# Kernel tuning notes

Hardware: AMD Instinct MI355X
Metric: run time of the kernel (lower is better)

## Reference

```python
import jax, jax.numpy as jnp
import numpy as np

B, M, E, H = 256, 196, 1024, 8
Dh = E // H          # 128 = att_mid_dim[0]
MID = 64             # att_mid_dim[1]
ALPHA = 1.3          # CELU alpha
EPS = 1e-5


def group_norm(x, w, b, groups=H, eps=EPS):
    # x: [N, C]; torch GroupNorm over channel groups
    N, C = x.shape
    xg = x.reshape(N, groups, C // groups)
    mu = xg.mean(-1, keepdims=True)
    var = xg.var(-1, keepdims=True)
    xn = ((xg - mu) * jax.lax.rsqrt(var + eps)).reshape(N, C)
    return xn * w + b


def proj(x, W, b, gw, gb):
    # Linear -> CELU(1.3) -> GroupNorm(H)
    return group_norm(jax.nn.celu(x @ W + b, alpha=ALPHA), gw, gb)


def setup_inputs() -> dict:
    key0 = jax.random.key(0)
    ks = jax.random.split(key0, 16)
    d = {}
    d["query"] = jax.random.normal(ks[0], (B, E), jnp.float32)
    d["key"] = jax.random.normal(ks[1], (B, M, E), jnp.float32)
    d["mask"] = jax.random.randint(ks[2], (B, M), 0, 2, jnp.int32)
    d["value1"] = jax.random.normal(ks[3], (B, E), jnp.float32)
    d["value2"] = jax.random.normal(ks[4], (B, M, E), jnp.float32)
    s = 0.02
    for i, nm in enumerate(["q", "k", "v1", "v2"]):
        d[f"W{nm}"] = jax.random.normal(ks[5 + i], (E, E), jnp.float32) * s
        d[f"b{nm}"] = jnp.zeros((E,), jnp.float32)
        d[f"g{nm}_w"] = jnp.ones((E,), jnp.float32)
        d[f"g{nm}_b"] = jnp.zeros((E,), jnp.float32)
    d["Wb"] = jax.random.normal(ks[9], (Dh, MID), jnp.float32) * s
    d["bb"] = jnp.zeros((MID,), jnp.float32)
    d["Ws"] = jax.random.normal(ks[10], (MID, 1), jnp.float32) * s
    d["bs"] = jnp.zeros((1,), jnp.float32)
    d["Wc"] = jax.random.normal(ks[11], (MID, Dh), jnp.float32) * s
    d["bc"] = jnp.zeros((Dh,), jnp.float32)
    return d


def reference(query, key, mask, value1, value2,
              Wq, bq, gq_w, gq_b, Wk, bk, gk_w, gk_b,
              Wv1, bv1, gv1_w, gv1_b, Wv2, bv2, gv2_w, gv2_b,
              Wb, bb, Ws, bs, Wc, bc):
    # input projections (dropout layers are identity at eval)
    q = proj(query, Wq, bq, gq_w, gq_b).reshape(B, H, Dh)
    v1 = proj(value1, Wv1, bv1, gv1_w, gv1_b).reshape(B, H, Dh)
    k = proj(key.reshape(-1, E), Wk, bk, gk_w, gk_b).reshape(B, M, H, Dh).transpose(0, 2, 1, 3)   # [B,H,M,Dh]
    v2 = proj(value2.reshape(-1, E), Wv2, bv2, gv2_w, gv2_b).reshape(B, M, H, Dh).transpose(0, 2, 1, 3)

    # SCAttDec
    att_map = q[:, :, None, :] * k                                # [B,H,M,Dh]
    hidden = jax.nn.relu(att_map @ Wb + bb)                       # [B,H,M,MID]
    maskf = mask.astype(hidden.dtype)                             # [B,M]
    mext = maskf[:, None, :, None]                                # [B,1,M,1]
    att_map_pool = jnp.sum(hidden * mext, axis=2) / jnp.sum(mext, axis=2)   # [B,H,MID]

    alpha_spatial = (hidden @ Ws + bs)[..., 0]                    # [B,H,M]
    alpha_spatial = jnp.where(mask[:, None, :] == 0, -1e9, alpha_spatial)
    alpha_spatial = jax.nn.softmax(alpha_spatial, axis=-1)
    v2_pooled = jnp.einsum("bhm,bhmd->bhd", alpha_spatial, v2)    # [B,H,Dh]

    alpha_channel = jax.nn.sigmoid(att_map_pool @ Wc + bc)        # [B,H,Dh]
    attn = v1 * v2_pooled * alpha_channel                         # [B,H,Dh]
    return attn.reshape(B, H * Dh)
```

## Files before the change

kernel.cpp:

```cpp
#include <hip/hip_runtime.h>

typedef unsigned short u16;
typedef unsigned int u32;
typedef unsigned long long u64;
typedef __attribute__((ext_vector_type(8))) short short8;
typedef __attribute__((ext_vector_type(4))) float floatx4;

#define E_ 1024
#define B_ 256
#define M_ 196
#define H_ 8
#define DH_ 128
#define MID_ 64
#define NKROW 50176

__device__ __forceinline__ u16 f2bf(float f){
  union { float f; u32 u; } v; v.f = f;
  return (u16)((v.u + (((v.u >> 16) & 1u) + 0x7fffu)) >> 16);
}
__device__ __forceinline__ float bf2f(u16 h){
  union { u32 u; float f; } v; v.u = ((u32)h) << 16;
  return v.f;
}
__device__ __forceinline__ u32 pack_bf2(float a, float b){
  u32 ua = __float_as_uint(a) + 0x8000u;
  u32 ub = __float_as_uint(b) + 0x8000u;
  return __builtin_amdgcn_perm(ub, ua, 0x07060302);
}
__device__ __forceinline__ void gl_lds16(const void* g, void* l){
  __builtin_amdgcn_global_load_lds(
      (const __attribute__((address_space(1))) u32*)g,
      (__attribute__((address_space(3))) u32*)l, 16, 0, 0);
}

__global__ __launch_bounds__(256) void xconv_kernel(
    float* __restrict__ key, float* __restrict__ value2,
    float* __restrict__ query, float* __restrict__ value1)
{
  int gr = blockIdx.x * 8 + (threadIdx.x >> 5);
  int i  = threadIdx.x & 31;
  float* X; int r;
  if (gr < NKROW)               { X = key;    r = gr; }
  else if (gr < 2*NKROW)        { X = value2; r = gr - NKROW; }
  else if (gr < 2*NKROW + B_)   { X = query;  r = gr - 2*NKROW; }
  else                          { X = value1; r = gr - 2*NKROW - B_; }
  const float4* src = (const float4*)(X + (size_t)r * E_) + i * 8;
  float4 v[8];
  #pragma unroll
  for (int j = 0; j < 8; j++) v[j] = src[j];
  __syncthreads();
  uint4 o[4];
  #pragma unroll
  for (int j = 0; j < 4; j++){
    o[j].x = pack_bf2(v[2*j].x,   v[2*j].y);
    o[j].y = pack_bf2(v[2*j].z,   v[2*j].w);
    o[j].z = pack_bf2(v[2*j+1].x, v[2*j+1].y);
    o[j].w = pack_bf2(v[2*j+1].z, v[2*j+1].w);
  }
  uint4* dst = (uint4*)((u16*)X + (size_t)r * 2048) + i * 4;
  #pragma unroll
  for (int j = 0; j < 4; j++) dst[j] = o[j];
}

__global__ __launch_bounds__(256) void wconv_kernel(
    const float* __restrict__ Wq, const float* __restrict__ Wk,
    const float* __restrict__ Wv1, const float* __restrict__ Wv2,
    u16* __restrict__ Wt)
{
  __shared__ u16 tile[64][72];
  const float* W = (blockIdx.z == 0) ? Wq : (blockIdx.z == 1) ? Wk
                 : (blockIdx.z == 2) ? Wv1 : Wv2;
  u16* out = Wt + (size_t)blockIdx.z * (E_ * E_);
  int k0 = blockIdx.x * 64, c0 = blockIdx.y * 64;
  int tx = threadIdx.x & 63, ty = threadIdx.x >> 6;
  #pragma unroll
  for (int i = 0; i < 16; i++){
    int k = ty * 16 + i;
    tile[k][tx] = f2bf(W[(size_t)(k0 + k) * E_ + c0 + tx]);
  }
  __syncthreads();
  #pragma unroll
  for (int i = 0; i < 16; i++){
    int c = ty * 16 + i;
    out[(size_t)(c0 + c) * E_ + k0 + tx] = tile[tx][c];
  }
}

__global__ __launch_bounds__(256) void proj_kernel(
    const u16* __restrict__ xq_, const u16* __restrict__ xk_,
    const u16* __restrict__ xv1_, const u16* __restrict__ xv2_,
    const float* __restrict__ bq, const float* __restrict__ gqw, const float* __restrict__ gqb,
    const float* __restrict__ bk, const float* __restrict__ gkw, const float* __restrict__ gkb,
    const float* __restrict__ bv1, const float* __restrict__ gv1w, const float* __restrict__ gv1b,
    const float* __restrict__ bv2, const float* __restrict__ gv2w, const float* __restrict__ gv2b,
    const u16* __restrict__ Wt,
    u16* __restrict__ qout, u16* __restrict__ khead,
    u16* __restrict__ v1out, u16* __restrict__ v2head)
{
  __shared__ __align__(16) u16 a_lds[128 * 64];
  __shared__ __align__(16) u16 b_lds[128 * 64];
  __shared__ float s_sum[256];
  __shared__ float s_sq[256];

  const int tid = threadIdx.x;
  const int w = tid >> 6, lane = tid & 63, qd = lane >> 4, lr = lane & 15;
  const int rh = w >> 1, ch = w & 1;

  const int mtb = blockIdx.y;
  const u16* X; const float *bias, *gw, *gb; u16* outp; int row0, matsel, hm;
  if (mtb < 392)      { X = xk_;  bias = bk;  gw = gkw;  gb = gkb;  outp = khead;  row0 = mtb*128;        matsel = 1; hm = 1; }
  else if (mtb < 784) { X = xv2_; bias = bv2; gw = gv2w; gb = gv2b; outp = v2head; row0 = (mtb-392)*128;  matsel = 3; hm = 1; }
  else if (mtb < 786) { X = xq_;  bias = bq;  gw = gqw;  gb = gqb;  outp = qout;   row0 = (mtb-784)*128;  matsel = 0; hm = 0; }
  else                { X = xv1_; bias = bv1; gw = gv1w; gb = gv1b; outp = v1out;  row0 = (mtb-786)*128;  matsel = 2; hm = 0; }
  const int hsel = blockIdx.x, col0 = hsel * 128;

  const int sl = lane & 7, sr = lane >> 3, swc = sl ^ sr;
  const u16* aptr = X + (size_t)(row0 + w*32 + sr) * 2048 + swc * 8;
  const u16* bptr = Wt + (size_t)matsel * (E_*E_) + (size_t)(col0 + w*32 + sr) * E_ + swc * 8;

  floatx4 acc[4][4];
  #pragma unroll
  for (int i = 0; i < 4; i++)
    #pragma unroll
    for (int j = 0; j < 4; j++){
      floatx4 z = {0.f, 0.f, 0.f, 0.f};
      acc[i][j] = z;
    }

  for (int kt = 0; kt < 16; kt++){
    __syncthreads();
    #pragma unroll
    for (int c = 0; c < 4; c++)
      gl_lds16(aptr + (size_t)c*8*2048 + kt*64, &a_lds[(w*32 + c*8)*64]);
    #pragma unroll
    for (int c = 0; c < 4; c++)
      gl_lds16(bptr + (size_t)c*8*E_ + kt*64, &b_lds[(w*32 + c*8)*64]);
    __syncthreads();
    #pragma unroll
    for (int ks = 0; ks < 2; ks++){
      const int slot = ((ks*4 + qd) ^ (lr & 7)) * 8;
      short8 afr[4], bfr[4];
      #pragma unroll
      for (int m2 = 0; m2 < 4; m2++)
        afr[m2] = *(const short8*)&a_lds[(rh*64 + m2*16 + lr)*64 + slot];
      #pragma unroll
      for (int nt = 0; nt < 4; nt++)
        bfr[nt] = *(const short8*)&b_lds[(ch*64 + nt*16 + lr)*64 + slot];
      #pragma unroll
      for (int m2 = 0; m2 < 4; m2++)
        #pragma unroll
        for (int nt = 0; nt < 4; nt++)
          acc[m2][nt] = __builtin_amdgcn_mfma_f32_16x16x32_bf16(afr[m2], bfr[nt], acc[m2][nt], 0, 0, 0);
    }
  }

  float biasv[4], gwv[4], gbv[4];
  #pragma unroll
  for (int nt = 0; nt < 4; nt++){
    int c = col0 + ch*64 + nt*16 + lr;
    biasv[nt] = bias[c]; gwv[nt] = gw[c]; gbv[nt] = gb[c];
  }
  #pragma unroll
  for (int m2 = 0; m2 < 4; m2++){
    #pragma unroll
    for (int r = 0; r < 4; r++){
      float s = 0.f, s2 = 0.f;
      #pragma unroll
      for (int nt = 0; nt < 4; nt++){
        float x = acc[m2][nt][r] + biasv[nt];
        x = (x > 0.f) ? x : 1.3f * expm1f(x * (1.0f / 1.3f));
        acc[m2][nt][r] = x;
        s += x; s2 += x * x;
      }
      #pragma unroll
      for (int off = 1; off < 16; off <<= 1){
        s  += __shfl_xor(s,  off, 64);
        s2 += __shfl_xor(s2, off, 64);
      }
      if (lr == 0){
        int row = rh*64 + m2*16 + qd*4 + r;
        s_sum[row*2 + ch] = s;
        s_sq [row*2 + ch] = s2;
      }
    }
  }
  __syncthreads();
  #pragma unroll
  for (int m2 = 0; m2 < 4; m2++){
    #pragma unroll
    for (int r = 0; r < 4; r++){
      int row = rh*64 + m2*16 + qd*4 + r;
      float s  = s_sum[row*2] + s_sum[row*2 + 1];
      float s2 = s_sq [row*2] + s_sq [row*2 + 1];
      float mean = s * 0.0078125f;
      float var  = s2 * 0.0078125f - mean * mean;
      float rstd = rsqrtf(var + 1e-5f);
      u32 rg = row0 + row;
      size_t base;
      if (hm){
        u32 bi = (u32)(((u64)rg * 171197ull) >> 25);
        u32 m  = rg - bi * 196u;
        base = ((size_t)(bi*H_ + hsel)*M_ + m) * DH_ + ch*64;
      } else {
        base = (size_t)rg * E_ + col0 + ch*64;
      }
      #pragma unroll
      for (int nt = 0; nt < 4; nt++)
        outp[base + nt*16 + lr] = f2bf((acc[m2][nt][r] - mean) * rstd * gwv[nt] + gbv[nt]);
    }
  }
}

__global__ __launch_bounds__(256) void attn_kernel(
    const u16* __restrict__ qproj, const u16* __restrict__ khead,
    const u16* __restrict__ v1proj, const u16* __restrict__ v2head,
    const int* __restrict__ mask,
    const float* __restrict__ Wb, const float* __restrict__ bb,
    const float* __restrict__ Ws, const float* __restrict__ bs,
    const float* __restrict__ Wc, const float* __restrict__ bc,
    float* __restrict__ outp)
{
  __shared__ u16 wbt[64 * 136];
  __shared__ float qv[128];
  __shared__ float mrow[208];
  __shared__ float logitv[208];
  __shared__ float hsum_l[4][64];
  __shared__ float wexpv[208];
  __shared__ float poolv[64];
  __shared__ float v2acc[4][128];
  __shared__ float red[8];

  const int tid = threadIdx.x;
  const int w = tid >> 6, lane = tid & 63, qd = lane >> 4, lr = lane & 15;
  const int b = blockIdx.y, h = blockIdx.x;

  const u16* kbase  = khead  + (size_t)(b*H_ + h) * (M_*DH_);
  const u16* v2base = v2head + (size_t)(b*H_ + h) * (M_*DH_);

  if (tid < 128) qv[tid] = bf2f(qproj[(size_t)b * E_ + h * DH_ + tid]);
  if (tid < 208) mrow[tid] = (tid < M_) ? (float)mask[b * M_ + tid] : 0.f;
  __syncthreads();

  {
    int n = tid & 63, kb = (tid >> 6) * 32;
    #pragma unroll
    for (int kk = 0; kk < 32; kk++)
      wbt[n * 136 + kb + kk] = f2bf(qv[kb + kk] * Wb[(kb + kk) * MID_ + n]);
  }
  __syncthreads();

  float wsv[4], bbv[4];
  #pragma unroll
  for (int nt = 0; nt < 4; nt++){ wsv[nt] = Ws[nt * 16 + lr]; bbv[nt] = bb[nt * 16 + lr]; }
  const float bsv = bs[0];
  float hs[4] = {0, 0, 0, 0};

  for (int mt = w; mt < 13; mt += 4){
    int mrow_g = mt * 16 + lr;
    int mcl = (mrow_g < M_) ? mrow_g : (M_ - 1);
    const u16* arow = kbase + (size_t)mcl * DH_;
    floatx4 hacc[4];
    #pragma unroll
    for (int nt = 0; nt < 4; nt++){ floatx4 z = {0.f, 0.f, 0.f, 0.f}; hacc[nt] = z; }
    #pragma unroll
    for (int kc = 0; kc < 4; kc++){
      short8 afr = *(const short8*)(arow + kc * 32 + qd * 8);
      #pragma unroll
      for (int nt = 0; nt < 4; nt++){
        short8 bfr = *(const short8*)&wbt[(nt * 16 + lr) * 136 + kc * 32 + qd * 8];
        hacc[nt] = __builtin_amdgcn_mfma_f32_16x16x32_bf16(afr, bfr, hacc[nt], 0, 0, 0);
      }
    }
    float lp[4] = {0, 0, 0, 0};
    #pragma unroll
    for (int nt = 0; nt < 4; nt++){
      #pragma unroll
      for (int r = 0; r < 4; r++){
        float hv = hacc[nt][r] + bbv[nt];
        hv = fmaxf(hv, 0.f);
        lp[r] += hv * wsv[nt];
        hs[nt] += mrow[mt * 16 + qd * 4 + r] * hv;
      }
    }
    #pragma unroll
    for (int r = 0; r < 4; r++){
      float a = lp[r];
      #pragma unroll
      for (int off = 1; off < 16; off <<= 1) a += __shfl_xor(a, off, 64);
      if (lr == 0) logitv[mt * 16 + qd * 4 + r] = a + bsv;
    }
  }
  #pragma unroll
  for (int nt = 0; nt < 4; nt++){
    hs[nt] += __shfl_xor(hs[nt], 16, 64);
    hs[nt] += __shfl_xor(hs[nt], 32, 64);
  }
  if (lane < 16){
    #pragma unroll
    for (int nt = 0; nt < 4; nt++) hsum_l[w][nt * 16 + lane] = hs[nt];
  }
  __syncthreads();

  if (w == 0){
    float s = 0.f;
    for (int m = lane; m < M_; m += 64) s += mrow[m];
    #pragma unroll
    for (int off = 1; off < 64; off <<= 1) s += __shfl_xor(s, off, 64);
    if (lane == 0) red[0] = s;
  } else if (w == 1){
    float mx = -1e30f;
    for (int m = lane; m < M_; m += 64) if (mrow[m] > 0.5f) mx = fmaxf(mx, logitv[m]);
    #pragma unroll
    for (int off = 1; off < 64; off <<= 1) mx = fmaxf(mx, __shfl_xor(mx, off, 64));
    if (lane == 0) red[1] = mx;
  } else if (w == 2){
    poolv[lane & 63] = hsum_l[0][lane & 63] + hsum_l[1][lane & 63]
                     + hsum_l[2][lane & 63] + hsum_l[3][lane & 63];
  }
  __syncthreads();
  const float cnt = red[0], mx = red[1];
  if (tid < 208)
    wexpv[tid] = (tid < M_ && mrow[tid] > 0.5f) ? expf(logitv[tid] - mx) : 0.f;
  __syncthreads();
  if (w == 0){
    float s = 0.f;
    for (int m = lane; m < M_; m += 64) s += wexpv[m];
    #pragma unroll
    for (int off = 1; off < 64; off <<= 1) s += __shfl_xor(s, off, 64);
    if (lane == 0) red[2] = s;
  } else if (w == 1){
    poolv[lane & 63] = poolv[lane & 63] / cnt;
  }
  __syncthreads();
  const float S = red[2];

  {
    float ac[8] = {0, 0, 0, 0, 0, 0, 0, 0};
    #pragma unroll
    for (int it = 0; it < 13; it++){
      int m = it * 16 + w * 4 + qd;
      if (m < M_){
        float we = wexpv[m];
        uint4 u = *(const uint4*)(v2base + (size_t)m * DH_ + lr * 8);
        ac[0] += we * bf2f((u16)(u.x & 0xffff));
        ac[1] += we * bf2f((u16)(u.x >> 16));
        ac[2] += we * bf2f((u16)(u.y & 0xffff));
        ac[3] += we * bf2f((u16)(u.y >> 16));
        ac[4] += we * bf2f((u16)(u.z & 0xffff));
        ac[5] += we * bf2f((u16)(u.z >> 16));
        ac[6] += we * bf2f((u16)(u.w & 0xffff));
        ac[7] += we * bf2f((u16)(u.w >> 16));
      }
    }
    #pragma unroll
    for (int j = 0; j < 8; j++){
      ac[j] += __shfl_xor(ac[j], 16, 64);
      ac[j] += __shfl_xor(ac[j], 32, 64);
    }
    if (qd == 0){
      #pragma unroll
      for (int j = 0; j < 8; j++) v2acc[w][lr * 8 + j] = ac[j];
    }
  }
  __syncthreads();

  if (tid < 128){
    float a = 0.f;
    #pragma unroll 8
    for (int j = 0; j < 64; j++) a += poolv[j] * Wc[j * DH_ + tid];
    float acv = 1.f / (1.f + expf(-(a + bc[tid])));
    float vp = (v2acc[0][tid] + v2acc[1][tid] + v2acc[2][tid] + v2acc[3][tid]) / S;
    float o = bf2f(v1proj[(size_t)b * E_ + h * DH_ + tid]) * vp * acv;
    outp[(size_t)b * E_ + h * DH_ + tid] = o;
  }
}

extern "C" void kernel_launch(void* const* d_in, const int* in_sizes, int n_in,
                              void* d_out, int out_size, void* d_ws, size_t ws_size,
                              hipStream_t stream)
{
  float* query  = (float*)d_in[0];
  float* key    = (float*)d_in[1];
  const int* mask = (const int*)d_in[2];
  float* value1 = (float*)d_in[3];
  float* value2 = (float*)d_in[4];
  const float* Wq  = (const float*)d_in[5];
  const float* bq  = (const float*)d_in[6];
  const float* gqw = (const float*)d_in[7];
  const float* gqb = (const float*)d_in[8];
  const float* Wk  = (const float*)d_in[9];
  const float* bk  = (const float*)d_in[10];
  const float* gkw = (const float*)d_in[11];
  const float* gkb = (const float*)d_in[12];
  const float* Wv1 = (const float*)d_in[13];
  const float* bv1 = (const float*)d_in[14];
  const float* gv1w= (const float*)d_in[15];
  const float* gv1b= (const float*)d_in[16];
  const float* Wv2 = (const float*)d_in[17];
  const float* bv2 = (const float*)d_in[18];
  const float* gv2w= (const float*)d_in[19];
  const float* gv2b= (const float*)d_in[20];
  const float* Wb  = (const float*)d_in[21];
  const float* bb  = (const float*)d_in[22];
  const float* Ws  = (const float*)d_in[23];
  const float* bs  = (const float*)d_in[24];
  const float* Wc  = (const float*)d_in[25];
  const float* bc  = (const float*)d_in[26];

  const size_t NHD = (size_t)B_ * H_ * M_ * DH_;
  u16* khead  = (u16*)d_ws;
  u16* v2head = khead  + NHD;
  u16* qout   = v2head + NHD;
  u16* v1out  = qout   + (size_t)B_ * E_;
  u16* Wt     = v1out  + (size_t)B_ * E_;

  xconv_kernel<<<(2*NKROW + 2*B_)/8, 256, 0, stream>>>(key, value2, query, value1);

  dim3 g0(16, 16, 4);
  wconv_kernel<<<g0, 256, 0, stream>>>(Wq, Wk, Wv1, Wv2, Wt);

  dim3 g1(8, 788);
  proj_kernel<<<g1, 256, 0, stream>>>(
      (const u16*)query, (const u16*)key, (const u16*)value1, (const u16*)value2,
      bq, gqw, gqb, bk, gkw, gkb, bv1, gv1w, gv1b, bv2, gv2w, gv2b,
      Wt, qout, khead, v1out, v2head);

  dim3 g2(H_, B_);
  attn_kernel<<<g2, 256, 0, stream>>>(qout, khead, v1out, v2head, mask,
      Wb, bb, Ws, bs, Wc, bc, (float*)d_out);
}
```

Before: 1.020 ms.

## Enlarge projection GEMM tile to 256x256 with double-buffered LDS prefetch

The projection GEMM moves from 128x128 tiles with 256 threads to 256x256 tiles with 512 threads. K steps of 32 now use double-buffered LDS, so the next tile's global-to-LDS load overlaps the current MFMAs, and each wave owns a full 128-column head, which removes the cross-wave LDS reduction for GroupNorm. This is meant to raise data reuse per loaded byte and hide load latency, at the cost of more accumulator registers per thread. The other changes are smaller: the xconv loads are made coalesced, CELU and the softmax/sigmoid exponentials use fast __expf, and the Wc matvec is split across all 256 threads.

```diff
diff --git a/kernel.cpp b/kernel.cpp
--- a/kernel.cpp
+++ b/kernel.cpp
@@ -31,6 +31,10 @@
   __builtin_amdgcn_global_load_lds(
       (const __attribute__((address_space(1))) u32*)g,
       (__attribute__((address_space(3))) u32*)l, 16, 0, 0);
+}
+__device__ __forceinline__ float celu_f(float x){
+  float xn = 1.3f * (__expf(x * 0.76923076923f) - 1.0f);
+  return x > 0.f ? x : xn;
 }
 
 __global__ __launch_bounds__(256) void xconv_kernel(
@@ -44,22 +48,19 @@
   else if (gr < 2*NKROW)        { X = value2; r = gr - NKROW; }
   else if (gr < 2*NKROW + B_)   { X = query;  r = gr - 2*NKROW; }
   else                          { X = value1; r = gr - 2*NKROW - B_; }
-  const float4* src = (const float4*)(X + (size_t)r * E_) + i * 8;
+  const float4* src = (const float4*)(X + (size_t)r * E_);
   float4 v[8];
   #pragma unroll
-  for (int j = 0; j < 8; j++) v[j] = src[j];
-  __syncthreads();
-  uint4 o[4];
-  #pragma unroll
-  for (int j = 0; j < 4; j++){
-    o[j].x = pack_bf2(v[2*j].x,   v[2*j].y);
-    o[j].y = pack_bf2(v[2*j].z,   v[2*j].w);
-    o[j].z = pack_bf2(v[2*j+1].x, v[2*j+1].y);
-    o[j].w = pack_bf2(v[2*j+1].z, v[2*j+1].w);
-  }
-  uint4* dst = (uint4*)((u16*)X + (size_t)r * 2048) + i * 4;
-  #pragma unroll
-  for (int j = 0; j < 4; j++) dst[j] = o[j];
+  for (int j = 0; j < 8; j++) v[j] = src[j * 32 + i];
+  __syncthreads();
+  uint2* dst = (uint2*)((u16*)X + (size_t)r * 2048);
+  #pragma unroll
+  for (int j = 0; j < 8; j++){
+    uint2 o;
+    o.x = pack_bf2(v[j].x, v[j].y);
+    o.y = pack_bf2(v[j].z, v[j].w);
+    dst[j * 32 + i] = o;
+  }
 }
 
 __global__ __launch_bounds__(256) void wconv_kernel(
@@ -86,7 +87,7 @@
   }
 }
 
-__global__ __launch_bounds__(256) void proj_kernel(
+__global__ __launch_bounds__(512, 2) void proj_kernel(
     const u16* __restrict__ xq_, const u16* __restrict__ xk_,
     const u16* __restrict__ xv1_, const u16* __restrict__ xv2_,
     const float* __restrict__ bq, const float* __restrict__ gqw, const float* __restrict__ gqb,
@@ -97,78 +98,83 @@
     u16* __restrict__ qout, u16* __restrict__ khead,
     u16* __restrict__ v1out, u16* __restrict__ v2head)
 {
-  __shared__ __align__(16) u16 a_lds[128 * 64];
-  __shared__ __align__(16) u16 b_lds[128 * 64];
-  __shared__ float s_sum[256];
-  __shared__ float s_sq[256];
+  __shared__ __align__(16) u16 a_lds[2][256 * 32];
+  __shared__ __align__(16) u16 b_lds[2][256 * 32];
 
   const int tid = threadIdx.x;
   const int w = tid >> 6, lane = tid & 63, qd = lane >> 4, lr = lane & 15;
-  const int rh = w >> 1, ch = w & 1;
-
-  const int mtb = blockIdx.y;
+  const int wm = w & 3, wn = w >> 2;
+
+  const int mtb = blockIdx.x;
   const u16* X; const float *bias, *gw, *gb; u16* outp; int row0, matsel, hm;
-  if (mtb < 392)      { X = xk_;  bias = bk;  gw = gkw;  gb = gkb;  outp = khead;  row0 = mtb*128;        matsel = 1; hm = 1; }
-  else if (mtb < 784) { X = xv2_; bias = bv2; gw = gv2w; gb = gv2b; outp = v2head; row0 = (mtb-392)*128;  matsel = 3; hm = 1; }
-  else if (mtb < 786) { X = xq_;  bias = bq;  gw = gqw;  gb = gqb;  outp = qout;   row0 = (mtb-784)*128;  matsel = 0; hm = 0; }
-  else                { X = xv1_; bias = bv1; gw = gv1w; gb = gv1b; outp = v1out;  row0 = (mtb-786)*128;  matsel = 2; hm = 0; }
-  const int hsel = blockIdx.x, col0 = hsel * 128;
-
-  const int sl = lane & 7, sr = lane >> 3, swc = sl ^ sr;
-  const u16* aptr = X + (size_t)(row0 + w*32 + sr) * 2048 + swc * 8;
-  const u16* bptr = Wt + (size_t)matsel * (E_*E_) + (size_t)(col0 + w*32 + sr) * E_ + swc * 8;
-
-  floatx4 acc[4][4];
+  if (mtb < 196)      { X = xk_;  bias = bk;  gw = gkw;  gb = gkb;  outp = khead;  row0 = mtb*256;        matsel = 1; hm = 1; }
+  else if (mtb < 392) { X = xv2_; bias = bv2; gw = gv2w; gb = gv2b; outp = v2head; row0 = (mtb-196)*256;  matsel = 3; hm = 1; }
+  else if (mtb == 392){ X = xq_;  bias = bq;  gw = gqw;  gb = gqb;  outp = qout;   row0 = 0;              matsel = 0; hm = 0; }
+  else                { X = xv1_; bias = bv1; gw = gv1w; gb = gv1b; outp = v1out;  row0 = 0;              matsel = 2; hm = 0; }
+  const int cp = blockIdx.y, col0 = cp * 256;
+
+  const int srow = lane >> 2, sslot = lane & 3, sswz = sslot ^ (srow & 3);
+  const u16* aptr0 = X + (size_t)(row0 + (w*2    )*16 + srow) * 2048 + sswz * 8;
+  const u16* aptr1 = X + (size_t)(row0 + (w*2 + 1)*16 + srow) * 2048 + sswz * 8;
+  const u16* wbase = Wt + (size_t)matsel * (E_*E_);
+  const u16* bptr0 = wbase + (size_t)(col0 + (w*2    )*16 + srow) * E_ + sswz * 8;
+  const u16* bptr1 = wbase + (size_t)(col0 + (w*2 + 1)*16 + srow) * E_ + sswz * 8;
+
+  floatx4 acc[4][8];
   #pragma unroll
   for (int i = 0; i < 4; i++)
     #pragma unroll
-    for (int j = 0; j < 4; j++){
+    for (int j = 0; j < 8; j++){
       floatx4 z = {0.f, 0.f, 0.f, 0.f};
       acc[i][j] = z;
     }
 
-  for (int kt = 0; kt < 16; kt++){
+  gl_lds16(aptr0, &a_lds[0][(w*2    )*16*32]);
+  gl_lds16(aptr1, &a_lds[0][(w*2 + 1)*16*32]);
+  gl_lds16(bptr0, &b_lds[0][(w*2    )*16*32]);
+  gl_lds16(bptr1, &b_lds[0][(w*2 + 1)*16*32]);
+  __syncthreads();
+
+  const int fslot = (qd ^ (lr & 3)) * 8;
+  for (int kt = 0; kt < 32; kt++){
+    const int cur = kt & 1, nxt = cur ^ 1;
+    if (kt < 31){
+      const int ko = (kt + 1) * 32;
+      gl_lds16(aptr0 + ko, &a_lds[nxt][(w*2    )*16*32]);
+      gl_lds16(aptr1 + ko, &a_lds[nxt][(w*2 + 1)*16*32]);
+      gl_lds16(bptr0 + ko, &b_lds[nxt][(w*2    )*16*32]);
+      gl_lds16(bptr1 + ko, &b_lds[nxt][(w*2 + 1)*16*32]);
+    }
+    short8 afr[4], bfr[8];
+    #pragma unroll
+    for (int m2 = 0; m2 < 4; m2++)
+      afr[m2] = *(const short8*)&a_lds[cur][(wm*64 + m2*16 + lr)*32 + fslot];
+    #pragma unroll
+    for (int nt = 0; nt < 8; nt++)
+      bfr[nt] = *(const short8*)&b_lds[cur][(wn*128 + nt*16 + lr)*32 + fslot];
+    #pragma unroll
+    for (int m2 = 0; m2 < 4; m2++)
+      #pragma unroll
+      for (int nt = 0; nt < 8; nt++)
+        acc[m2][nt] = __builtin_amdgcn_mfma_f32_16x16x32_bf16(afr[m2], bfr[nt], acc[m2][nt], 0, 0, 0);
     __syncthreads();
-    #pragma unroll
-    for (int c = 0; c < 4; c++)
-      gl_lds16(aptr + (size_t)c*8*2048 + kt*64, &a_lds[(w*32 + c*8)*64]);
-    #pragma unroll
-    for (int c = 0; c < 4; c++)
-      gl_lds16(bptr + (size_t)c*8*E_ + kt*64, &b_lds[(w*32 + c*8)*64]);
-    __syncthreads();
-    #pragma unroll
-    for (int ks = 0; ks < 2; ks++){
-      const int slot = ((ks*4 + qd) ^ (lr & 7)) * 8;
-      short8 afr[4], bfr[4];
-      #pragma unroll
-      for (int m2 = 0; m2 < 4; m2++)
-        afr[m2] = *(const short8*)&a_lds[(rh*64 + m2*16 + lr)*64 + slot];
-      #pragma unroll
-      for (int nt = 0; nt < 4; nt++)
-        bfr[nt] = *(const short8*)&b_lds[(ch*64 + nt*16 + lr)*64 + slot];
-      #pragma unroll
-      for (int m2 = 0; m2 < 4; m2++)
-        #pragma unroll
-        for (int nt = 0; nt < 4; nt++)
-          acc[m2][nt] = __builtin_amdgcn_mfma_f32_16x16x32_bf16(afr[m2], bfr[nt], acc[m2][nt], 0, 0, 0);
-    }
-  }
-
-  float biasv[4], gwv[4], gbv[4];
-  #pragma unroll
-  for (int nt = 0; nt < 4; nt++){
-    int c = col0 + ch*64 + nt*16 + lr;
+  }
+
+  float biasv[8], gwv[8], gbv[8];
+  #pragma unroll
+  for (int nt = 0; nt < 8; nt++){
+    int c = col0 + wn*128 + nt*16 + lr;
     biasv[nt] = bias[c]; gwv[nt] = gw[c]; gbv[nt] = gb[c];
   }
+  const int head = cp*2 + wn;
   #pragma unroll
   for (int m2 = 0; m2 < 4; m2++){
     #pragma unroll
     for (int r = 0; r < 4; r++){
       float s = 0.f, s2 = 0.f;
       #pragma unroll
-      for (int nt = 0; nt < 4; nt++){
-        float x = acc[m2][nt][r] + biasv[nt];
-        x = (x > 0.f) ? x : 1.3f * expm1f(x * (1.0f / 1.3f));
+      for (int nt = 0; nt < 8; nt++){
+        float x = celu_f(acc[m2][nt][r] + biasv[nt]);
         acc[m2][nt][r] = x;
         s += x; s2 += x * x;
       }
@@ -177,35 +183,20 @@
         s  += __shfl_xor(s,  off, 64);
         s2 += __shfl_xor(s2, off, 64);
       }
-      if (lr == 0){
-        int row = rh*64 + m2*16 + qd*4 + r;
-        s_sum[row*2 + ch] = s;
-        s_sq [row*2 + ch] = s2;
-      }
-    }
-  }
-  __syncthreads();
-  #pragma unroll
-  for (int m2 = 0; m2 < 4; m2++){
-    #pragma unroll
-    for (int r = 0; r < 4; r++){
-      int row = rh*64 + m2*16 + qd*4 + r;
-      float s  = s_sum[row*2] + s_sum[row*2 + 1];
-      float s2 = s_sq [row*2] + s_sq [row*2 + 1];
       float mean = s * 0.0078125f;
       float var  = s2 * 0.0078125f - mean * mean;
       float rstd = rsqrtf(var + 1e-5f);
-      u32 rg = row0 + row;
+      u32 rg = row0 + wm*64 + m2*16 + qd*4 + r;
       size_t base;
       if (hm){
         u32 bi = (u32)(((u64)rg * 171197ull) >> 25);
         u32 m  = rg - bi * 196u;
-        base = ((size_t)(bi*H_ + hsel)*M_ + m) * DH_ + ch*64;
+        base = ((size_t)(bi*H_ + head)*M_ + m) * DH_;
       } else {
-        base = (size_t)rg * E_ + col0 + ch*64;
-      }
-      #pragma unroll
-      for (int nt = 0; nt < 4; nt++)
+        base = (size_t)rg * E_ + head * DH_;
+      }
+      #pragma unroll
+      for (int nt = 0; nt < 8; nt++)
         outp[base + nt*16 + lr] = f2bf((acc[m2][nt][r] - mean) * rstd * gwv[nt] + gbv[nt]);
     }
   }
@@ -228,6 +219,7 @@
   __shared__ float wexpv[208];
   __shared__ float poolv[64];
   __shared__ float v2acc[4][128];
+  __shared__ float wc2[2][128];
   __shared__ float red[8];
 
   const int tid = threadIdx.x;
@@ -320,7 +312,7 @@
   __syncthreads();
   const float cnt = red[0], mx = red[1];
   if (tid < 208)
-    wexpv[tid] = (tid < M_ && mrow[tid] > 0.5f) ? expf(logitv[tid] - mx) : 0.f;
+    wexpv[tid] = (tid < M_ && mrow[tid] > 0.5f) ? __expf(logitv[tid] - mx) : 0.f;
   __syncthreads();
   if (w == 0){
     float s = 0.f;
@@ -364,11 +356,18 @@
   }
   __syncthreads();
 
-  if (tid < 128){
+  {
+    int d = tid & 127, jh = tid >> 7;
     float a = 0.f;
     #pragma unroll 8
-    for (int j = 0; j < 64; j++) a += poolv[j] * Wc[j * DH_ + tid];
-    float acv = 1.f / (1.f + expf(-(a + bc[tid])));
+    for (int j = jh * 32; j < jh * 32 + 32; j++) a += poolv[j] * Wc[j * DH_ + d];
+    wc2[jh][d] = a;
+  }
+  __syncthreads();
+
+  if (tid < 128){
+    float a = wc2[0][tid] + wc2[1][tid];
+    float acv = 1.f / (1.f + __expf(-(a + bc[tid])));
     float vp = (v2acc[0][tid] + v2acc[1][tid] + v2acc[2][tid] + v2acc[3][tid]) / S;
     float o = bf2f(v1proj[(size_t)b * E_ + h * DH_ + tid]) * vp * acv;
     outp[(size_t)b * E_ + h * DH_ + tid] = o;
@@ -419,8 +418,8 @@
   dim3 g0(16, 16, 4);
   wconv_kernel<<<g0, 256, 0, stream>>>(Wq, Wk, Wv1, Wv2, Wt);
 
-  dim3 g1(8, 788);
-  proj_kernel<<<g1, 256, 0, stream>>>(
+  dim3 g1(394, 4);
+  proj_kernel<<<g1, 512, 0, stream>>>(
       (const u16*)query, (const u16*)key, (const u16*)value1, (const u16*)value2,
       bq, gqw, gqb, bk, gkw, gkb, bv1, gv1w, gv1b, bv2, gv2w, gv2b,
       Wt, qout, khead, v1out, v2head);
```

New measurement: 924.0 us. 9.4% less time.
